# Optimization experiments

Hardware: AMD Instinct MI355X
Metric: run time of the kernel (lower is better)

## Reference

```python
import jax, jax.numpy as jnp
import numpy as np

# Dims: B=4 batch, S=1024 seq, E=512 embed_dim, H=8 heads, K=3 gate lookback.
_B, _S, _E, _H, _K = 4, 1024, 512, 8, 3
_EPS_LN = 1e-5
_DIV_DELTA = 1e-12


def setup_inputs() -> dict:
    key = jax.random.key(0)
    ks = jax.random.split(key, 8)

    def w(k, shape, s=0.02):
        return jax.random.normal(k, shape, jnp.float32) * s

    return {
        "query": jax.random.normal(ks[0], (_B, _S, _E), jnp.float32),
        "ln1_g": jnp.ones((_E,), jnp.float32),
        "ln1_b": jnp.zeros((_E,), jnp.float32),
        "in_proj_w": w(ks[1], (3 * _E, _E)),          # packed W_q;W_k;W_v
        "in_proj_b": jnp.zeros((3 * _E,), jnp.float32),
        "out_w": w(ks[2], (_E, _H * _E)),             # out_proj: Linear(E*H -> E)
        "out_b": jnp.zeros((_E,), jnp.float32),
        "conv_w": w(ks[3], (_H, _E, _K)),             # SyntacticDistanceGate causal conv
        "conv_b": jnp.zeros((_H,), jnp.float32),
        "ln2_g": jnp.ones((_E,), jnp.float32),
        "ln2_b": jnp.zeros((_E,), jnp.float32),
        "mlp_w1": w(ks[4], (4 * _E, _E)),
        "mlp_b1": jnp.zeros((4 * _E,), jnp.float32),
        "mlp_w2": w(ks[5], (_E, 4 * _E)),
        "mlp_b2": jnp.zeros((_E,), jnp.float32),
    }


def _layer_norm(x, g, b):
    m = jnp.mean(x, axis=-1, keepdims=True)
    v = jnp.mean(jnp.square(x - m), axis=-1, keepdims=True)
    return (x - m) * jax.lax.rsqrt(v + _EPS_LN) * g + b


def _syntactic_gate(x, conv_w, conv_b):
    """x: [B,S,E] -> gate [B,H,S,S], distance [B,H,S].
    Causal depth-to-head conv produces per-head syntactic distances; gate is a
    smooth comparison sigmoid(d_i - d_j) (PRPN-style distance gating)."""
    K = conv_w.shape[-1]
    xp = jnp.pad(x, ((0, 0), (K - 1, 0), (0, 0)))  # causal left pad
    S = x.shape[1]
    d = conv_b[None, :, None]
    for k in range(K):  # tiny fixed lookback loop
        d = d + jnp.einsum("bse,he->bhs", xp[:, k:k + S, :], conv_w[:, :, k])
    distance = jnp.tanh(d)                               # [B,H,S]
    gate = jax.nn.sigmoid(distance[:, :, :, None] - distance[:, :, None, :])
    return gate, distance


def reference(query, ln1_g, ln1_b, in_proj_w, in_proj_b, out_w, out_b,
              conv_w, conv_b, ln2_g, ln2_b, mlp_w1, mlp_b1, mlp_w2, mlp_b2):
    B, S, E = query.shape
    H = conv_w.shape[0]

    nq = _layer_norm(query, ln1_g, ln1_b)  # self-attention: key=value=normed query

    gate, _distance = _syntactic_gate(nq, conv_w, conv_b)  # [B,H,S,S]

    # In-projections (heads are NOT split: each head sees full E-dim q/k/v).
    qkv = nq @ in_proj_w.T + in_proj_b          # [B,S,3E]
    q, k, v = jnp.split(qkv, 3, axis=-1)

    # Raw scores (scaled by sqrt(E), per source). Identical across heads since
    # q/k are merely repeated per head; compute once and broadcast over H.
    scores = jnp.einsum("bie,bje->bij", q, k) / jnp.sqrt(jnp.float32(E))

    # NOTE: with no key_padding_mask the source skips softmax entirely; the
    # gate multiplies RAW scores, then sum-normalizes.
    w = scores[:, None, :, :] * gate                       # [B,H,S,S]
    w = w / (jnp.sum(w, axis=-1, keepdims=True) + _DIV_DELTA)

    ctx = jnp.einsum("bhij,bje->bhie", w, v)               # [B,H,S,E]
    # torch: chunk over head-major dim 0 then cat on features -> [B,S,H*E]
    ctx = jnp.transpose(ctx, (0, 2, 1, 3)).reshape(B, S, H * E)
    attn_out = ctx @ out_w.T + out_b                       # [B,S,E]

    x = query + attn_out                                   # layer_scale_1 = Identity
    h = _layer_norm(x, ln2_g, ln2_b)
    h = jax.nn.gelu(h @ mlp_w1.T + mlp_b1, approximate=False)
    x = x + (h @ mlp_w2.T + mlp_b2)                        # layer_scale_2 = Identity
    return x
```

## Files before the change

### kernel.cpp

```cpp
#include <hip/hip_runtime.h>
#include <math.h>

#define SQ 1024
#define EE 512
#define NB 4
#define NH 8

typedef __attribute__((ext_vector_type(8))) short bfrag;
typedef __attribute__((ext_vector_type(4))) float f32x4;
typedef __attribute__((ext_vector_type(4))) unsigned short u16x4;
typedef __attribute__((ext_vector_type(8))) unsigned short u16x8;

typedef __attribute__((address_space(3))) unsigned int lds_u32;
typedef const __attribute__((address_space(1))) unsigned int glb_u32;

__device__ __forceinline__ float sep(float x) {
  asm volatile("" : "+v"(x));
  return x;
}

__device__ __forceinline__ unsigned short f2bf(float f) {
  unsigned u = __builtin_bit_cast(unsigned, f);
  unsigned r = (u + 0x7fffu + ((u >> 16) & 1u)) >> 16;
  return (unsigned short)r;
}
__device__ __forceinline__ float bf2f(unsigned short h) {
  unsigned u = ((unsigned)h) << 16;
  return __builtin_bit_cast(float, u);
}

__device__ __forceinline__ void split4(float4 v, u16x4& h, u16x4& l) {
  h.x = f2bf(v.x); l.x = f2bf(v.x - bf2f(h.x));
  h.y = f2bf(v.y); l.y = f2bf(v.y - bf2f(h.y));
  h.z = f2bf(v.z); l.z = f2bf(v.z - bf2f(h.z));
  h.w = f2bf(v.w); l.w = f2bf(v.w - bf2f(h.w));
}

__device__ __forceinline__ int swzi(int row, int c8) {
  return row * 40 + ((c8 ^ ((row >> 2) & 6)) << 2);
}

__global__ __launch_bounds__(64) void ln_np(const float* __restrict__ x,
                                            const float* __restrict__ g,
                                            const float* __restrict__ b,
                                            float* __restrict__ y) {
  __shared__ float xs[EE];
  __shared__ float bc[2];
  long long t = blockIdx.x;
  int lane = threadIdx.x;
#pragma unroll
  for (int m = 0; m < 8; m++) xs[lane + 64 * m] = x[t * EE + lane + 64 * m];
  __syncthreads();
  int l = lane >> 3, a = lane & 7;
  float r = 0.f;
  if (lane < 32) {
    r = xs[l * 128 + a];
#pragma unroll
    for (int m = 1; m < 16; m++) r = r + xs[l * 128 + 8 * m + a];
  }
  r = r + __shfl_xor(r, 1);
  r = r + __shfl_xor(r, 2);
  r = r + __shfl_xor(r, 4);
  r = r + __shfl_xor(r, 8);
  r = r + __shfl_xor(r, 16);
  if (lane == 0) bc[0] = r / 512.0f;
  __syncthreads();
  float mean = bc[0];
  r = 0.f;
  if (lane < 32) {
#pragma unroll
    for (int m = 0; m < 16; m++) {
      float d = sep(xs[l * 128 + 8 * m + a] - mean);
      float s2 = sep(d * d);
      r = (m == 0) ? s2 : (r + s2);
    }
  }
  r = r + __shfl_xor(r, 1);
  r = r + __shfl_xor(r, 2);
  r = r + __shfl_xor(r, 4);
  r = r + __shfl_xor(r, 8);
  r = r + __shfl_xor(r, 16);
  if (lane == 0) bc[1] = r / 512.0f;
  __syncthreads();
  float var = bc[1];
  float rs = 1.0f / sqrtf(var + 1e-5f);
#pragma unroll
  for (int m = 0; m < 8; m++) {
    int i = lane + 64 * m;
    float d = sep(xs[i] - mean);
    float t1 = sep(d * rs);
    float t2 = sep(t1 * g[i]);
    y[t * EE + i] = t2 + b[i];
  }
}

__global__ __launch_bounds__(64) void ln_np_s(const float* __restrict__ x,
                                              const float* __restrict__ g,
                                              const float* __restrict__ b,
                                              unsigned short* __restrict__ yh,
                                              unsigned short* __restrict__ yl) {
  __shared__ float xs[EE];
  __shared__ float bc[2];
  long long t = blockIdx.x;
  int lane = threadIdx.x;
#pragma unroll
  for (int m = 0; m < 8; m++) xs[lane + 64 * m] = x[t * EE + lane + 64 * m];
  __syncthreads();
  int l = lane >> 3, a = lane & 7;
  float r = 0.f;
  if (lane < 32) {
    r = xs[l * 128 + a];
#pragma unroll
    for (int m = 1; m < 16; m++) r = r + xs[l * 128 + 8 * m + a];
  }
  r = r + __shfl_xor(r, 1);
  r = r + __shfl_xor(r, 2);
  r = r + __shfl_xor(r, 4);
  r = r + __shfl_xor(r, 8);
  r = r + __shfl_xor(r, 16);
  if (lane == 0) bc[0] = r / 512.0f;
  __syncthreads();
  float mean = bc[0];
  r = 0.f;
  if (lane < 32) {
#pragma unroll
    for (int m = 0; m < 16; m++) {
      float d = sep(xs[l * 128 + 8 * m + a] - mean);
      float s2 = sep(d * d);
      r = (m == 0) ? s2 : (r + s2);
    }
  }
  r = r + __shfl_xor(r, 1);
  r = r + __shfl_xor(r, 2);
  r = r + __shfl_xor(r, 4);
  r = r + __shfl_xor(r, 8);
  r = r + __shfl_xor(r, 16);
  if (lane == 0) bc[1] = r / 512.0f;
  __syncthreads();
  float var = bc[1];
  float rs = 1.0f / sqrtf(var + 1e-5f);
#pragma unroll
  for (int m = 0; m < 8; m++) {
    int i = lane + 64 * m;
    float d = sep(xs[i] - mean);
    float t1 = sep(d * rs);
    float t2 = sep(t1 * g[i]);
    float o = t2 + b[i];
    unsigned short hh = f2bf(o);
    yh[t * EE + i] = hh;
    yl[t * EE + i] = f2bf(o - bf2f(hh));
  }
}

__global__ __launch_bounds__(256) void dist_np(const float* __restrict__ nq,
                                               const float* __restrict__ conv_w,
                                               const float* __restrict__ conv_b,
                                               float* __restrict__ dist) {
  int bh = blockIdx.x;
  int b = bh >> 3, h = bh & 7;
  float cb = conv_b[h];
  const float* W = conv_w + (long long)h * EE * 3;
  int s = blockIdx.y * 256 + threadIdx.x;
  float d = cb;
#pragma unroll
  for (int k = 0; k < 3; k++) {
    int t = s - 2 + k;
    if (t < 0) continue;
    const float* row = nq + ((long long)b * SQ + t) * EE;
    float acc = 0.f;
    for (int e = 0; e < EE; e++) acc = __builtin_fmaf(row[e], W[e * 3 + k], acc);
    d = sep(d + acc);
  }
  dist[(long long)bh * SQ + s] = (float)tanh((double)d);
}

__device__ __forceinline__ float gelu_exact(float x) {
  return 0.5f * x * (1.f + erff(x / 1.41421356237309504880f));
}

template <int ACT, int SPLITK>
__global__ __launch_bounds__(256) void gemm_nt(const float* __restrict__ A, int lda, long long sA,
                                               const float* __restrict__ B, int ldb, long long sB,
                                               const float* __restrict__ bias,
                                               const float* __restrict__ Res,
                                               float* __restrict__ C, int ldc, long long sC,
                                               int K, float alpha) {
  __shared__ float As[16][68];
  __shared__ float Bs[16][68];
  int z = blockIdx.z;
  A += (long long)z * sA;
  B += (long long)z * sB;
  C += (long long)z * sC;
  int m0 = blockIdx.y * 64, n0 = blockIdx.x * 64;
  int tid = threadIdx.x;
  int lr = tid >> 2, lc = tid & 3;
  int tx = tid & 15, ty = tid >> 4;
  float acc[4][4] = {};
  float acc2[4][4] = {};
  const float* Arow = A + (long long)(m0 + lr) * lda + lc * 4;
  const float* Brow = B + (long long)(n0 + lr) * ldb + lc * 4;
  float4 a4 = *(const float4*)(Arow);
  float4 b4 = *(const float4*)(Brow);
  for (int k0 = 0; k0 < K; k0 += 16) {
    __syncthreads();
    As[lc * 4 + 0][lr] = a4.x; As[lc * 4 + 1][lr] = a4.y;
    As[lc * 4 + 2][lr] = a4.z; As[lc * 4 + 3][lr] = a4.w;
    Bs[lc * 4 + 0][lr] = b4.x; Bs[lc * 4 + 1][lr] = b4.y;
    Bs[lc * 4 + 2][lr] = b4.z; Bs[lc * 4 + 3][lr] = b4.w;
    __syncthreads();
    int kn = (k0 + 16 < K) ? (k0 + 16) : k0;
    float4 a4n = *(const float4*)(Arow + kn);
    float4 b4n = *(const float4*)(Brow + kn);
    float(*tgt)[4] = (SPLITK > 0 && k0 >= SPLITK) ? acc2 : acc;
#pragma unroll
    for (int kk = 0; kk < 16; kk++) {
      float4 av = *(const float4*)&As[kk][ty * 4];
      float4 bv = *(const float4*)&Bs[kk][tx * 4];
      float a[4] = {av.x, av.y, av.z, av.w};
      float bb[4] = {bv.x, bv.y, bv.z, bv.w};
#pragma unroll
      for (int i = 0; i < 4; i++)
#pragma unroll
        for (int j = 0; j < 4; j++) tgt[i][j] += a[i] * bb[j];
    }
    a4 = a4n;
    b4 = b4n;
  }
  if (SPLITK > 0) {
#pragma unroll
    for (int i = 0; i < 4; i++)
#pragma unroll
      for (int j = 0; j < 4; j++) acc[i][j] = sep(acc[i][j]) + acc2[i][j];
  }
  float4 bias4 = make_float4(0.f, 0.f, 0.f, 0.f);
  if (ACT != 2 && bias) bias4 = *(const float4*)(bias + n0 + tx * 4);
#pragma unroll
  for (int i = 0; i < 4; i++) {
    int row = m0 + ty * 4 + i;
    float o[4];
    if (ACT == 2) {
#pragma unroll
      for (int j = 0; j < 4; j++) o[j] = acc[i][j] / alpha;
    } else {
      o[0] = sep(acc[i][0] * alpha) + bias4.x;
      o[1] = sep(acc[i][1] * alpha) + bias4.y;
      o[2] = sep(acc[i][2] * alpha) + bias4.z;
      o[3] = sep(acc[i][3] * alpha) + bias4.w;
    }
    if (ACT == 1) {
#pragma unroll
      for (int j = 0; j < 4; j++) o[j] = gelu_exact(o[j]);
    }
    if (Res) {
      float4 r4 = *(const float4*)(Res + (long long)row * ldc + n0 + tx * 4);
      o[0] = sep(o[0]) + r4.x; o[1] = sep(o[1]) + r4.y;
      o[2] = sep(o[2]) + r4.z; o[3] = sep(o[3]) + r4.w;
    }
    *(float4*)(C + (long long)row * ldc + n0 + tx * 4) = make_float4(o[0], o[1], o[2], o[3]);
  }
}

__global__ __launch_bounds__(64) void rowsum_np(const float* __restrict__ scores,
                                                const float* __restrict__ dist,
                                                float* __restrict__ invrs) {
  __shared__ float wsm[SQ];
  int i = blockIdx.x;
  int z = blockIdx.y;
  int b = z >> 3;
  const float* srow = scores + ((long long)b * SQ + i) * SQ;
  const float* dz = dist + (long long)z * SQ;
  float di = dz[i];
  int lane = threadIdx.x;
#pragma unroll
  for (int m = 0; m < 16; m++) {
    int j = lane + 64 * m;
    float e = (float)exp((double)(dz[j] - di));
    float gg = 1.f / (1.f + e);
    wsm[j] = srow[j] * gg;
  }
  __syncthreads();
  int l = lane >> 3, a = lane & 7;
  float r = wsm[l * 128 + a];
#pragma unroll
  for (int m = 1; m < 16; m++) r = r + wsm[l * 128 + 8 * m + a];
  r = r + __shfl_xor(r, 1);
  r = r + __shfl_xor(r, 2);
  r = r + __shfl_xor(r, 4);
  r = r + __shfl_xor(r, 8);
  r = r + __shfl_xor(r, 16);
  r = r + __shfl_xor(r, 32);
  if (lane == 0) invrs[(long long)z * SQ + i] = 1.f / (r + 1e-12f);
}

__global__ __launch_bounds__(256) void vsplit_t(const float* __restrict__ qkv,
                                                unsigned short* __restrict__ VhT,
                                                unsigned short* __restrict__ VlT) {
  __shared__ float tile[64][65];
  int b = blockIdx.z;
  int j0 = blockIdx.x * 64;
  int e0 = blockIdx.y * 64;
  const float* V = qkv + (long long)b * SQ * (3 * EE) + 2 * EE;
  unsigned short* Vh = VhT + (long long)b * EE * SQ;
  unsigned short* Vl = VlT + (long long)b * EE * SQ;
  int tx = threadIdx.x & 15, ty = threadIdx.x >> 4;
#pragma unroll
  for (int r = 0; r < 4; r++) {
    int j = j0 + ty + r * 16;
    float4 v = *(const float4*)(V + (long long)j * (3 * EE) + e0 + tx * 4);
    tile[ty + r * 16][tx * 4 + 0] = v.x;
    tile[ty + r * 16][tx * 4 + 1] = v.y;
    tile[ty + r * 16][tx * 4 + 2] = v.z;
    tile[ty + r * 16][tx * 4 + 3] = v.w;
  }
  __syncthreads();
#pragma unroll
  for (int r = 0; r < 4; r++) {
    int el = ty + r * 16;
    float4 f;
    f.x = tile[tx * 4 + 0][el];
    f.y = tile[tx * 4 + 1][el];
    f.z = tile[tx * 4 + 2][el];
    f.w = tile[tx * 4 + 3][el];
    u16x4 hh, ll;
    split4(f, hh, ll);
    long long o = (long long)(e0 + el) * SQ + j0 + tx * 4;
    *(u16x4*)(Vh + o) = hh;
    *(u16x4*)(Vl + o) = ll;
  }
}

__global__ __launch_bounds__(256) void wsplit(const float* __restrict__ W,
                                              unsigned short* __restrict__ Wh,
                                              unsigned short* __restrict__ Wl, int n4) {
  int i = blockIdx.x * 256 + threadIdx.x;
  if (i >= n4) return;
  float4 v = *(const float4*)(W + (long long)i * 4);
  u16x4 h, l;
  split4(v, h, l);
  *(u16x4*)(Wh + (long long)i * 4) = h;
  *(u16x4*)(Wl + (long long)i * 4) = l;
}

__global__ __launch_bounds__(256) void ctx_bf3(const float* __restrict__ scores,
                                               const float* __restrict__ dist,
                                               const float* __restrict__ invrs,
                                               const unsigned short* __restrict__ VhT,
                                               const unsigned short* __restrict__ VlT,
                                               unsigned short* __restrict__ Ch,
                                               unsigned short* __restrict__ Cl) {
  __shared__ __align__(16) unsigned short Ah[128 * 40], Al[128 * 40];
  __shared__ __align__(16) unsigned short Bh[128 * 40], Bl[128 * 40];
  int z = blockIdx.z, b = z >> 3, h = z & 7;
  const float* Sb = scores + (long long)b * SQ * SQ;
  const unsigned short* Vh = VhT + (long long)b * EE * SQ;
  const unsigned short* Vl = VlT + (long long)b * EE * SQ;
  unsigned short* Chb = Ch + (long long)b * SQ * (NH * EE) + h * EE;
  unsigned short* Clb = Cl + (long long)b * SQ * (NH * EE) + h * EE;
  const float* dz = dist + (long long)z * SQ;
  int m0 = blockIdx.y * 128, n0 = blockIdx.x * 128;
  int tid = threadIdx.x;
  int wave = tid >> 6, lane = tid & 63;
  int quad = lane >> 4, l16 = lane & 15;
  f32x4 acc[4][4];
#pragma unroll
  for (int mf = 0; mf < 4; mf++)
#pragma unroll
    for (int nf = 0; nf < 4; nf++) acc[mf][nf] = (f32x4)(0.f);

  int aam = tid & 127, aakc = tid >> 7;
  float di = dz[m0 + aam];
  float inv = invrs[(long long)z * SQ + m0 + aam];
  const float* Srow = Sb + (long long)(m0 + aam) * SQ;
  int brow = tid & 127, bk8 = tid >> 7;
  const unsigned short* VhRow = Vh + (long long)(n0 + brow) * SQ;
  const unsigned short* VlRow = Vl + (long long)(n0 + brow) * SQ;

  u16x4 aH[4], aL[4];
  u16x8 bH[2], bL[2];

  auto loadconv = [&](int kb) {
#pragma unroll
    for (int r = 0; r < 4; r++) {
      int kc = aakc * 4 + r;
      float4 s4 = *(const float4*)(Srow + kb + kc * 4);
      float4 d4 = *(const float4*)(dz + kb + kc * 4);
      float4 a;
      a.x = (s4.x * __builtin_amdgcn_rcpf(1.f + __expf(d4.x - di))) * inv;
      a.y = (s4.y * __builtin_amdgcn_rcpf(1.f + __expf(d4.y - di))) * inv;
      a.z = (s4.z * __builtin_amdgcn_rcpf(1.f + __expf(d4.z - di))) * inv;
      a.w = (s4.w * __builtin_amdgcn_rcpf(1.f + __expf(d4.w - di))) * inv;
      split4(a, aH[r], aL[r]);
    }
#pragma unroll
    for (int r = 0; r < 2; r++) {
      bH[r] = *(const u16x8*)(VhRow + kb + (bk8 * 2 + r) * 8);
      bL[r] = *(const u16x8*)(VlRow + kb + (bk8 * 2 + r) * 8);
    }
  };

  loadconv(0);
  for (int k0 = 0; k0 < SQ; k0 += 32) {
    __syncthreads();
#pragma unroll
    for (int r = 0; r < 4; r++) {
      *(u16x4*)&Ah[swzi(aam, aakc * 4 + r)] = aH[r];
      *(u16x4*)&Al[swzi(aam, aakc * 4 + r)] = aL[r];
    }
#pragma unroll
    for (int r = 0; r < 2; r++) {
      *(u16x8*)&Bh[swzi(brow, (bk8 * 2 + r) * 2)] = bH[r];
      *(u16x8*)&Bl[swzi(brow, (bk8 * 2 + r) * 2)] = bL[r];
    }
    __syncthreads();
    int kn = (k0 + 32 < SQ) ? (k0 + 32) : k0;
    loadconv(kn);
    bfrag bhf[4], blf[4];
#pragma unroll
    for (int nf = 0; nf < 4; nf++) {
      int rb = (wave & 1) * 64 + nf * 16 + l16;
      bhf[nf] = *(const bfrag*)&Bh[swzi(rb, quad * 2)];
      blf[nf] = *(const bfrag*)&Bl[swzi(rb, quad * 2)];
    }
#pragma unroll
    for (int mf = 0; mf < 4; mf++) {
      int ra = (wave >> 1) * 64 + mf * 16 + l16;
      bfrag ah = *(const bfrag*)&Ah[swzi(ra, quad * 2)];
      bfrag al = *(const bfrag*)&Al[swzi(ra, quad * 2)];
#pragma unroll
      for (int nf = 0; nf < 4; nf++) {
        acc[mf][nf] = __builtin_amdgcn_mfma_f32_16x16x32_bf16(al, bhf[nf], acc[mf][nf], 0, 0, 0);
        acc[mf][nf] = __builtin_amdgcn_mfma_f32_16x16x32_bf16(ah, blf[nf], acc[mf][nf], 0, 0, 0);
        acc[mf][nf] = __builtin_amdgcn_mfma_f32_16x16x32_bf16(ah, bhf[nf], acc[mf][nf], 0, 0, 0);
      }
    }
  }
#pragma unroll
  for (int mf = 0; mf < 4; mf++) {
#pragma unroll
    for (int nf = 0; nf < 4; nf++) {
      int col = n0 + (wave & 1) * 64 + nf * 16 + l16;
#pragma unroll
      for (int r = 0; r < 4; r++) {
        int row = m0 + (wave >> 1) * 64 + mf * 16 + quad * 4 + r;
        float o = acc[mf][nf][r];
        unsigned short hh = f2bf(o);
        Chb[(long long)row * (NH * EE) + col] = hh;
        Clb[(long long)row * (NH * EE) + col] = f2bf(o - bf2f(hh));
      }
    }
  }
}

template <int ACT, int OUTM>
__global__ __launch_bounds__(256) void gemm_bf3w(
    const unsigned short* __restrict__ Ah_g, const unsigned short* __restrict__ Al_g, int lda,
    const unsigned short* __restrict__ Bh_g, const unsigned short* __restrict__ Bl_g, int ldb,
    const float* __restrict__ bias, const float* __restrict__ Res,
    float* __restrict__ C, unsigned short* __restrict__ Ch, unsigned short* __restrict__ Cl,
    int ldc, int K) {
  __shared__ __align__(16) unsigned short lds[3 * 12288];
  int gx = gridDim.x;
  int nwg = gx * (int)gridDim.y;
  int lin = blockIdx.y * gx + blockIdx.x;
  int cpx = nwg >> 3;
  int tl = (lin & 7) * cpx + (lin >> 3);
  int bx = tl % gx, by = tl / gx;
  int m0 = by * 128, n0 = bx * 64;
  int tid = threadIdx.x, wave = tid >> 6, lane = tid & 63;
  int quad = lane >> 4, l16 = lane & 15;

  const unsigned short* gptr[6];
  int ldsoff[6];
#pragma unroll
  for (int i = 0; i < 6; i++) {
    int d = wave * 6 + i;
    const unsigned short* src;
    int rowbase, ld, tb, qt;
    if (d < 8)       { src = Ah_g; rowbase = m0; ld = lda; tb = 0;     qt = d; }
    else if (d < 16) { src = Al_g; rowbase = m0; ld = lda; tb = 4096;  qt = d - 8; }
    else if (d < 20) { src = Bh_g; rowbase = n0; ld = ldb; tb = 8192;  qt = d - 16; }
    else             { src = Bl_g; rowbase = n0; ld = ldb; tb = 10240; qt = d - 20; }
    int row = qt * 16 + (lane >> 2);
    int cG = (lane & 3) ^ ((row >> 1) & 3);
    gptr[i] = src + (long long)(rowbase + row) * ld + cG * 8;
    ldsoff[i] = tb + qt * 512;
  }

  auto stage = [&](int buf, int kb) {
#pragma unroll
    for (int i = 0; i < 6; i++)
      __builtin_amdgcn_global_load_lds((glb_u32*)(gptr[i] + kb),
                                       (lds_u32*)&lds[buf * 12288 + ldsoff[i]], 16, 0, 0);
  };

  int aoff[4], boff[2];
#pragma unroll
  for (int mf = 0; mf < 4; mf++) {
    int r = (wave >> 1) * 64 + mf * 16 + l16;
    aoff[mf] = r * 32 + ((quad ^ ((r >> 1) & 3)) * 8);
  }
#pragma unroll
  for (int nf = 0; nf < 2; nf++) {
    int r = (wave & 1) * 32 + nf * 16 + l16;
    boff[nf] = r * 32 + ((quad ^ ((r >> 1) & 3)) * 8);
  }

  f32x4 acc[4][2];
#pragma unroll
  for (int mf = 0; mf < 4; mf++)
#pragma unroll
    for (int nf = 0; nf < 2; nf++) acc[mf][nf] = (f32x4)(0.f);

  int NT = K >> 5;
  stage(0, 0);
  stage(1, 32);
  int cur = 0;
  for (int t = 0; t < NT; t++) {
    int nb = cur + 2; if (nb >= 3) nb -= 3;
    int kf = (t + 2 < NT) ? (t + 2) * 32 : (NT - 1) * 32;
    stage(nb, kf);
    asm volatile("s_waitcnt vmcnt(12)" ::: "memory");
    __builtin_amdgcn_s_barrier();
    __builtin_amdgcn_sched_barrier(0);
    const unsigned short* L = &lds[cur * 12288];
    bfrag bh[2], bl[2];
#pragma unroll
    for (int nf = 0; nf < 2; nf++) {
      bh[nf] = *(const bfrag*)&L[8192 + boff[nf]];
      bl[nf] = *(const bfrag*)&L[10240 + boff[nf]];
    }
#pragma unroll
    for (int mf = 0; mf < 4; mf++) {
      bfrag ah = *(const bfrag*)&L[aoff[mf]];
      bfrag al = *(const bfrag*)&L[4096 + aoff[mf]];
#pragma unroll
      for (int nf = 0; nf < 2; nf++) {
        acc[mf][nf] = __builtin_amdgcn_mfma_f32_16x16x32_bf16(al, bh[nf], acc[mf][nf], 0, 0, 0);
        acc[mf][nf] = __builtin_amdgcn_mfma_f32_16x16x32_bf16(ah, bl[nf], acc[mf][nf], 0, 0, 0);
        acc[mf][nf] = __builtin_amdgcn_mfma_f32_16x16x32_bf16(ah, bh[nf], acc[mf][nf], 0, 0, 0);
      }
    }
    __builtin_amdgcn_sched_barrier(0);
    __builtin_amdgcn_s_barrier();
    cur++; if (cur >= 3) cur -= 3;
  }

#pragma unroll
  for (int mf = 0; mf < 4; mf++) {
#pragma unroll
    for (int nf = 0; nf < 2; nf++) {
      int col = n0 + (wave & 1) * 32 + nf * 16 + l16;
      float bi = bias ? bias[col] : 0.f;
#pragma unroll
      for (int r = 0; r < 4; r++) {
        int row = m0 + (wave >> 1) * 64 + mf * 16 + quad * 4 + r;
        float o = acc[mf][nf][r] + bi;
        if (ACT == 1) o = gelu_exact(o);
        if (OUTM == 0) {
          if (Res) o = o + Res[(long long)row * ldc + col];
          C[(long long)row * ldc + col] = o;
        } else {
          unsigned short hh = f2bf(o);
          Ch[(long long)row * ldc + col] = hh;
          Cl[(long long)row * ldc + col] = f2bf(o - bf2f(hh));
        }
      }
    }
  }
}

extern "C" void kernel_launch(void* const* d_in, const int* in_sizes, int n_in,
                              void* d_out, int out_size, void* d_ws, size_t ws_size,
                              hipStream_t stream) {
  const float* query     = (const float*)d_in[0];
  const float* ln1_g     = (const float*)d_in[1];
  const float* ln1_b     = (const float*)d_in[2];
  const float* in_proj_w = (const float*)d_in[3];
  const float* in_proj_b = (const float*)d_in[4];
  const float* out_w     = (const float*)d_in[5];
  const float* out_b     = (const float*)d_in[6];
  const float* conv_w    = (const float*)d_in[7];
  const float* conv_b    = (const float*)d_in[8];
  const float* ln2_g     = (const float*)d_in[9];
  const float* ln2_b     = (const float*)d_in[10];
  const float* mlp_w1    = (const float*)d_in[11];
  const float* mlp_b1    = (const float*)d_in[12];
  const float* mlp_w2    = (const float*)d_in[13];
  const float* mlp_b2    = (const float*)d_in[14];
  float* out = (float*)d_out;
  char* ws = (char*)d_ws;

  float* nq     = (float*)(ws + 0);
  float* qkv    = (float*)(ws + (8ull << 20));
  float* dist   = (float*)(ws + (32ull << 20));
  float* invrs  = (float*)(ws + (32ull << 20) + 131072);
  float* scores = (float*)(ws + (32ull << 20) + 262144);
  unsigned short* VhT = (unsigned short*)(ws + 0);
  unsigned short* VlT = (unsigned short*)(ws + (4ull << 20));
  unsigned short* ctxh = (unsigned short*)(ws + (48ull << 20) + 262144);
  unsigned short* ctxl = (unsigned short*)(ws + (80ull << 20) + 262144);
  unsigned short* out_wh = (unsigned short*)(ws + (32ull << 20) + 262144);
  unsigned short* out_wl = out_wh + 2097152;
  unsigned short* w1h    = out_wl + 2097152;
  unsigned short* w1l    = w1h + 1048576;
  unsigned short* w2h    = w1l + 1048576;
  unsigned short* w2l    = w2h + 1048576;
  unsigned short* ln2h = (unsigned short*)(ws + (48ull << 20) + 262144);
  unsigned short* ln2l = ln2h + 2097152;
  unsigned short* hbufh = (unsigned short*)(ws + 0);
  unsigned short* hbufl = hbufh + 8388608;

  ln_np<<<dim3(NB * SQ), 64, 0, stream>>>(query, ln1_g, ln1_b, nq);
  dist_np<<<dim3(NB * NH, 4), 256, 0, stream>>>(nq, conv_w, conv_b, dist);
  gemm_nt<0, 384><<<dim3(24, 64, 1), 256, 0, stream>>>(nq, EE, 0, in_proj_w, EE, 0,
                                                       in_proj_b, nullptr, qkv, 3 * EE, 0, EE, 1.f);
  vsplit_t<<<dim3(16, 8, NB), 256, 0, stream>>>(qkv, VhT, VlT);
  gemm_nt<2, 384><<<dim3(16, 16, NB), 256, 0, stream>>>(
      qkv, 3 * EE, (long long)SQ * 3 * EE, qkv + EE, 3 * EE, (long long)SQ * 3 * EE,
      nullptr, nullptr, scores, SQ, (long long)SQ * SQ, EE, sqrtf(512.0f));
  rowsum_np<<<dim3(SQ, NB * NH), 64, 0, stream>>>(scores, dist, invrs);
  ctx_bf3<<<dim3(4, 8, NB * NH), 256, 0, stream>>>(scores, dist, invrs, VhT, VlT,
                                                   ctxh, ctxl);
  wsplit<<<dim3(2048), 256, 0, stream>>>(out_w, out_wh, out_wl, 524288);
  wsplit<<<dim3(1024), 256, 0, stream>>>(mlp_w1, w1h, w1l, 262144);
  wsplit<<<dim3(1024), 256, 0, stream>>>(mlp_w2, w2h, w2l, 262144);
  gemm_bf3w<0, 0><<<dim3(8, 32), 256, 0, stream>>>(ctxh, ctxl, NH * EE, out_wh, out_wl, NH * EE,
                                                   out_b, query, out, nullptr, nullptr,
                                                   EE, NH * EE);
  ln_np_s<<<dim3(NB * SQ), 64, 0, stream>>>(out, ln2_g, ln2_b, ln2h, ln2l);
  gemm_bf3w<1, 1><<<dim3(32, 32), 256, 0, stream>>>(ln2h, ln2l, EE, w1h, w1l, EE,
                                                    mlp_b1, nullptr, nullptr, hbufh, hbufl,
                                                    4 * EE, EE);
  gemm_bf3w<0, 0><<<dim3(8, 32), 256, 0, stream>>>(hbufh, hbufl, 4 * EE, w2h, w2l, 4 * EE,
                                                   mlp_b2, out, out, nullptr, nullptr,
                                                   EE, 4 * EE);
}
```

Measured before the change: 730.1 us.

## Widen ctx tile to 128x256, precompute exp(distance), pack bf16 conversions

The context kernel's N tile doubles from 128 to 256, so each block reuses its gated-score A tile across twice as many V columns and the gate/normalize/split work per output halves. The sigmoid gate is rewritten algebraically as e_i/(e_i+e_j), using exp(distance) precomputed in the distance kernel and stored in the output buffer as scratch. This removes one exp per element from the inner load loop. The hi/lo bf16 split now uses the packed v_cvt_pk_bf16_f32 instruction. The costs are doubled accumulator registers and a larger LDS B tile, which may reduce occupancy (launch bounds request 2 blocks), and only 512 blocks are launched.

```diff
diff --git a/kernel.cpp b/kernel.cpp
--- a/kernel.cpp
+++ b/kernel.cpp
@@ -27,6 +27,13 @@
 __device__ __forceinline__ float bf2f(unsigned short h) {
   unsigned u = ((unsigned)h) << 16;
   return __builtin_bit_cast(float, u);
+}
+__device__ __forceinline__ float bitf(unsigned u) { return __builtin_bit_cast(float, u); }
+
+__device__ __forceinline__ unsigned cvtpk(float a, float b) {
+  unsigned r;
+  asm("v_cvt_pk_bf16_f32 %0, %1, %2" : "=v"(r) : "v"(a), "v"(b));
+  return r;
 }
 
 __device__ __forceinline__ void split4(float4 v, u16x4& h, u16x4& l) {
@@ -155,7 +162,8 @@
 __global__ __launch_bounds__(256) void dist_np(const float* __restrict__ nq,
                                                const float* __restrict__ conv_w,
                                                const float* __restrict__ conv_b,
-                                               float* __restrict__ dist) {
+                                               float* __restrict__ dist,
+                                               float* __restrict__ Edist) {
   int bh = blockIdx.x;
   int b = bh >> 3, h = bh & 7;
   float cb = conv_b[h];
@@ -171,7 +179,9 @@
     for (int e = 0; e < EE; e++) acc = __builtin_fmaf(row[e], W[e * 3 + k], acc);
     d = sep(d + acc);
   }
-  dist[(long long)bh * SQ + s] = (float)tanh((double)d);
+  float dv = (float)tanh((double)d);
+  dist[(long long)bh * SQ + s] = dv;
+  Edist[(long long)bh * SQ + s] = __expf(dv);
 }
 
 __device__ __forceinline__ float gelu_exact(float x) {
@@ -341,60 +351,65 @@
   *(u16x4*)(Wl + (long long)i * 4) = l;
 }
 
-__global__ __launch_bounds__(256) void ctx_bf3(const float* __restrict__ scores,
-                                               const float* __restrict__ dist,
-                                               const float* __restrict__ invrs,
-                                               const unsigned short* __restrict__ VhT,
-                                               const unsigned short* __restrict__ VlT,
-                                               unsigned short* __restrict__ Ch,
-                                               unsigned short* __restrict__ Cl) {
+__global__ __launch_bounds__(256, 2) void ctx_bf3(const float* __restrict__ scores,
+                                                  const float* __restrict__ Edist,
+                                                  const float* __restrict__ invrs,
+                                                  const unsigned short* __restrict__ VhT,
+                                                  const unsigned short* __restrict__ VlT,
+                                                  unsigned short* __restrict__ Ch,
+                                                  unsigned short* __restrict__ Cl) {
   __shared__ __align__(16) unsigned short Ah[128 * 40], Al[128 * 40];
-  __shared__ __align__(16) unsigned short Bh[128 * 40], Bl[128 * 40];
+  __shared__ __align__(16) unsigned short Bh[256 * 40], Bl[256 * 40];
   int z = blockIdx.z, b = z >> 3, h = z & 7;
   const float* Sb = scores + (long long)b * SQ * SQ;
   const unsigned short* Vh = VhT + (long long)b * EE * SQ;
   const unsigned short* Vl = VlT + (long long)b * EE * SQ;
   unsigned short* Chb = Ch + (long long)b * SQ * (NH * EE) + h * EE;
   unsigned short* Clb = Cl + (long long)b * SQ * (NH * EE) + h * EE;
-  const float* dz = dist + (long long)z * SQ;
-  int m0 = blockIdx.y * 128, n0 = blockIdx.x * 128;
+  const float* Ez = Edist + (long long)z * SQ;
+  int m0 = blockIdx.y * 128, n0 = blockIdx.x * 256;
   int tid = threadIdx.x;
   int wave = tid >> 6, lane = tid & 63;
   int quad = lane >> 4, l16 = lane & 15;
-  f32x4 acc[4][4];
+  f32x4 acc[4][8];
 #pragma unroll
   for (int mf = 0; mf < 4; mf++)
 #pragma unroll
-    for (int nf = 0; nf < 4; nf++) acc[mf][nf] = (f32x4)(0.f);
+    for (int nf = 0; nf < 8; nf++) acc[mf][nf] = (f32x4)(0.f);
 
   int aam = tid & 127, aakc = tid >> 7;
-  float di = dz[m0 + aam];
+  float ei = Ez[m0 + aam];
   float inv = invrs[(long long)z * SQ + m0 + aam];
+  float ci = ei * inv;
   const float* Srow = Sb + (long long)(m0 + aam) * SQ;
-  int brow = tid & 127, bk8 = tid >> 7;
+  int brow = tid;
   const unsigned short* VhRow = Vh + (long long)(n0 + brow) * SQ;
   const unsigned short* VlRow = Vl + (long long)(n0 + brow) * SQ;
 
-  u16x4 aH[4], aL[4];
-  u16x8 bH[2], bL[2];
+  uint2 aHp[4], aLp[4];
+  u16x8 bH[4], bL[4];
 
   auto loadconv = [&](int kb) {
 #pragma unroll
     for (int r = 0; r < 4; r++) {
       int kc = aakc * 4 + r;
       float4 s4 = *(const float4*)(Srow + kb + kc * 4);
-      float4 d4 = *(const float4*)(dz + kb + kc * 4);
-      float4 a;
-      a.x = (s4.x * __builtin_amdgcn_rcpf(1.f + __expf(d4.x - di))) * inv;
-      a.y = (s4.y * __builtin_amdgcn_rcpf(1.f + __expf(d4.y - di))) * inv;
-      a.z = (s4.z * __builtin_amdgcn_rcpf(1.f + __expf(d4.z - di))) * inv;
-      a.w = (s4.w * __builtin_amdgcn_rcpf(1.f + __expf(d4.w - di))) * inv;
-      split4(a, aH[r], aL[r]);
-    }
-#pragma unroll
-    for (int r = 0; r < 2; r++) {
-      bH[r] = *(const u16x8*)(VhRow + kb + (bk8 * 2 + r) * 8);
-      bL[r] = *(const u16x8*)(VlRow + kb + (bk8 * 2 + r) * 8);
+      float4 e4 = *(const float4*)(Ez + kb + kc * 4);
+      float ax = (s4.x * ci) * __builtin_amdgcn_rcpf(ei + e4.x);
+      float ay = (s4.y * ci) * __builtin_amdgcn_rcpf(ei + e4.y);
+      float az = (s4.z * ci) * __builtin_amdgcn_rcpf(ei + e4.z);
+      float aw = (s4.w * ci) * __builtin_amdgcn_rcpf(ei + e4.w);
+      unsigned h01 = cvtpk(ax, ay), h23 = cvtpk(az, aw);
+      float hx = bitf(h01 << 16), hy = bitf(h01 & 0xffff0000u);
+      float hz = bitf(h23 << 16), hw = bitf(h23 & 0xffff0000u);
+      unsigned l01 = cvtpk(ax - hx, ay - hy), l23 = cvtpk(az - hz, aw - hw);
+      aHp[r] = make_uint2(h01, h23);
+      aLp[r] = make_uint2(l01, l23);
+    }
+#pragma unroll
+    for (int c = 0; c < 4; c++) {
+      bH[c] = *(const u16x8*)(VhRow + kb + c * 8);
+      bL[c] = *(const u16x8*)(VlRow + kb + c * 8);
     }
   };
 
@@ -403,42 +418,42 @@
     __syncthreads();
 #pragma unroll
     for (int r = 0; r < 4; r++) {
-      *(u16x4*)&Ah[swzi(aam, aakc * 4 + r)] = aH[r];
-      *(u16x4*)&Al[swzi(aam, aakc * 4 + r)] = aL[r];
-    }
-#pragma unroll
-    for (int r = 0; r < 2; r++) {
-      *(u16x8*)&Bh[swzi(brow, (bk8 * 2 + r) * 2)] = bH[r];
-      *(u16x8*)&Bl[swzi(brow, (bk8 * 2 + r) * 2)] = bL[r];
+      *(uint2*)&Ah[swzi(aam, aakc * 4 + r)] = aHp[r];
+      *(uint2*)&Al[swzi(aam, aakc * 4 + r)] = aLp[r];
+    }
+#pragma unroll
+    for (int c = 0; c < 4; c++) {
+      *(u16x8*)&Bh[swzi(brow, 2 * c)] = bH[c];
+      *(u16x8*)&Bl[swzi(brow, 2 * c)] = bL[c];
     }
     __syncthreads();
     int kn = (k0 + 32 < SQ) ? (k0 + 32) : k0;
     loadconv(kn);
-    bfrag bhf[4], blf[4];
-#pragma unroll
-    for (int nf = 0; nf < 4; nf++) {
-      int rb = (wave & 1) * 64 + nf * 16 + l16;
-      bhf[nf] = *(const bfrag*)&Bh[swzi(rb, quad * 2)];
-      blf[nf] = *(const bfrag*)&Bl[swzi(rb, quad * 2)];
-    }
+    bfrag ah[4], al_[4];
 #pragma unroll
     for (int mf = 0; mf < 4; mf++) {
       int ra = (wave >> 1) * 64 + mf * 16 + l16;
-      bfrag ah = *(const bfrag*)&Ah[swzi(ra, quad * 2)];
-      bfrag al = *(const bfrag*)&Al[swzi(ra, quad * 2)];
-#pragma unroll
-      for (int nf = 0; nf < 4; nf++) {
-        acc[mf][nf] = __builtin_amdgcn_mfma_f32_16x16x32_bf16(al, bhf[nf], acc[mf][nf], 0, 0, 0);
-        acc[mf][nf] = __builtin_amdgcn_mfma_f32_16x16x32_bf16(ah, blf[nf], acc[mf][nf], 0, 0, 0);
-        acc[mf][nf] = __builtin_amdgcn_mfma_f32_16x16x32_bf16(ah, bhf[nf], acc[mf][nf], 0, 0, 0);
+      ah[mf] = *(const bfrag*)&Ah[swzi(ra, quad * 2)];
+      al_[mf] = *(const bfrag*)&Al[swzi(ra, quad * 2)];
+    }
+#pragma unroll
+    for (int nf = 0; nf < 8; nf++) {
+      int rb = (wave & 1) * 128 + nf * 16 + l16;
+      bfrag bh = *(const bfrag*)&Bh[swzi(rb, quad * 2)];
+      bfrag bl = *(const bfrag*)&Bl[swzi(rb, quad * 2)];
+#pragma unroll
+      for (int mf = 0; mf < 4; mf++) {
+        acc[mf][nf] = __builtin_amdgcn_mfma_f32_16x16x32_bf16(al_[mf], bh, acc[mf][nf], 0, 0, 0);
+        acc[mf][nf] = __builtin_amdgcn_mfma_f32_16x16x32_bf16(ah[mf], bl, acc[mf][nf], 0, 0, 0);
+        acc[mf][nf] = __builtin_amdgcn_mfma_f32_16x16x32_bf16(ah[mf], bh, acc[mf][nf], 0, 0, 0);
       }
     }
   }
 #pragma unroll
   for (int mf = 0; mf < 4; mf++) {
 #pragma unroll
-    for (int nf = 0; nf < 4; nf++) {
-      int col = n0 + (wave & 1) * 64 + nf * 16 + l16;
+    for (int nf = 0; nf < 8; nf++) {
+      int col = n0 + (wave & 1) * 128 + nf * 16 + l16;
 #pragma unroll
       for (int r = 0; r < 4; r++) {
         int row = m0 + (wave >> 1) * 64 + mf * 16 + quad * 4 + r;
@@ -609,9 +624,10 @@
   unsigned short* ln2l = ln2h + 2097152;
   unsigned short* hbufh = (unsigned short*)(ws + 0);
   unsigned short* hbufl = hbufh + 8388608;
+  float* Edist = (float*)d_out;
 
   ln_np<<<dim3(NB * SQ), 64, 0, stream>>>(query, ln1_g, ln1_b, nq);
-  dist_np<<<dim3(NB * NH, 4), 256, 0, stream>>>(nq, conv_w, conv_b, dist);
+  dist_np<<<dim3(NB * NH, 4), 256, 0, stream>>>(nq, conv_w, conv_b, dist, Edist);
   gemm_nt<0, 384><<<dim3(24, 64, 1), 256, 0, stream>>>(nq, EE, 0, in_proj_w, EE, 0,
                                                        in_proj_b, nullptr, qkv, 3 * EE, 0, EE, 1.f);
   vsplit_t<<<dim3(16, 8, NB), 256, 0, stream>>>(qkv, VhT, VlT);
@@ -619,8 +635,7 @@
       qkv, 3 * EE, (long long)SQ * 3 * EE, qkv + EE, 3 * EE, (long long)SQ * 3 * EE,
       nullptr, nullptr, scores, SQ, (long long)SQ * SQ, EE, sqrtf(512.0f));
   rowsum_np<<<dim3(SQ, NB * NH), 64, 0, stream>>>(scores, dist, invrs);
-  ctx_bf3<<<dim3(4, 8, NB * NH), 256, 0, stream>>>(scores, dist, invrs, VhT, VlT,
-                                                   ctxh, ctxl);
+  ctx_bf3<<<dim3(2, 8, NB * NH), 256, 0, stream>>>(scores, Edist, invrs, VhT, VlT, ctxh, ctxl);
   wsplit<<<dim3(2048), 256, 0, stream>>>(out_w, out_wh, out_wl, 524288);
   wsplit<<<dim3(1024), 256, 0, stream>>>(mlp_w1, w1h, w1l, 262144);
   wsplit<<<dim3(1024), 256, 0, stream>>>(mlp_w2, w2h, w2l, 262144);
```

Measured after the change: 669.4 us. 1.09x faster.
